# Optimization experiments

Hardware: AMD Instinct MI355X
Metric: run time of the kernel (lower is better)

The kernel has to match this reference:

```python
import math
import jax, jax.numpy as jnp
import numpy as np

D_MODEL = 512
N_HEADS = 8
FACTOR = 1
B, L = 16, 2048


def setup_inputs() -> dict:
    key = jax.random.key(0)
    ks = jax.random.split(key, 12)
    d = D_MODEL
    inp = {
        'queries': jax.random.normal(ks[0], (B, L, d), dtype=jnp.float32),
        'keys':    jax.random.normal(ks[1], (B, L, d), dtype=jnp.float32),
        'values':  jax.random.normal(ks[2], (B, L, d), dtype=jnp.float32),
        # projection params (nn.Linear: y = x @ W.T + b)
        'Wq': jax.random.normal(ks[3], (d, d), dtype=jnp.float32) * 0.02,
        'bq': jnp.zeros((d,), dtype=jnp.float32),
        'Wk': jax.random.normal(ks[4], (d, d), dtype=jnp.float32) * 0.02,
        'bk': jnp.zeros((d,), dtype=jnp.float32),
        'Wv': jax.random.normal(ks[5], (d, d), dtype=jnp.float32) * 0.02,
        'bv': jnp.zeros((d,), dtype=jnp.float32),
        'Wo': jax.random.normal(ks[6], (d, d), dtype=jnp.float32) * 0.02,
        'bo': jnp.zeros((d,), dtype=jnp.float32),
    }
    return inp


def _autocorrelation(q, k, v):
    # q, k, v: [B, H, E, L]
    length = q.shape[-1]
    q_fft = jnp.fft.rfft(q, axis=-1)
    k_fft = jnp.fft.rfft(k, axis=-1)
    corr = jnp.fft.irfft(q_fft * jnp.conj(k_fft), n=length, axis=-1)  # [B,H,E,L]

    # time_delay_agg_training
    top_k = int(FACTOR * math.log(length))  # static
    mean_value = corr.mean(axis=(1, 2))            # [B, L]
    _, index = jax.lax.top_k(mean_value.mean(axis=0), top_k)  # [k], batch-shared delays
    weights = mean_value[:, index]                 # [B, k]
    tmp_corr = jax.nn.softmax(weights, axis=-1)    # [B, k]

    # roll(values, -delay) == values[..., (arange(L)+delay) % L]
    idx = (jnp.arange(length)[None, :] + index[:, None]) % length  # [k, L]
    patterns = v[..., idx]                         # [B, H, E, k, L]
    delays_agg = jnp.einsum('bhekl,bk->bhel', patterns, tmp_corr)  # [B,H,E,L]
    return delays_agg


def reference(queries, keys, values, Wq, bq, Wk, bk, Wv, bv, Wo, bo):
    Bb, Ll, d = queries.shape
    H = N_HEADS
    E = d // H
    # projections, then [B, L, H, E] -> [B, H, E, L]
    q = (queries @ Wq.T + bq).reshape(Bb, Ll, H, E).transpose(0, 2, 3, 1)
    k = (keys    @ Wk.T + bk).reshape(Bb, Ll, H, E).transpose(0, 2, 3, 1)
    v = (values  @ Wv.T + bv).reshape(Bb, Ll, H, E).transpose(0, 2, 3, 1)

    agg = _autocorrelation(q, k, v)                 # [B, H, E, L]
    out = agg.transpose(0, 3, 1, 2).reshape(Bb, Ll, H * E)  # [B, L, d]
    return out @ Wo.T + bo
```

## Files before the change

kernel.cpp:

```cpp
#include <hip/hip_runtime.h>


typedef _Float16 f16;
typedef _Float16 f16x8 __attribute__((ext_vector_type(8)));
typedef _Float16 f16x4 __attribute__((ext_vector_type(4)));
typedef float    f32x4 __attribute__((ext_vector_type(4)));

#define PSI(i) ((i) + ((i) >> 3))
#define TWI(j) ((j) + ((j) >> 4))

__device__ __forceinline__ float2 f2add(float2 a, float2 b) { return make_float2(a.x + b.x, a.y + b.y); }
__device__ __forceinline__ float2 f2sub(float2 a, float2 b) { return make_float2(a.x - b.x, a.y - b.y); }
__device__ __forceinline__ float2 cmul(float2 a, float2 b)  { return make_float2(a.x * b.x - a.y * b.y, a.x * b.y + a.y * b.x); }

__global__ __launch_bounds__(256) void cvt_inputs(
    const float* __restrict__ q, const float* __restrict__ k, const float* __restrict__ v,
    f16* __restrict__ xq, f16* __restrict__ xk, f16* __restrict__ xv)
{
    const float* src = (blockIdx.y == 0) ? q : (blockIdx.y == 1) ? k : v;
    f16*         dst = (blockIdx.y == 0) ? xq : (blockIdx.y == 1) ? xk : xv;
    const int i = blockIdx.x * 256 + threadIdx.x;
    float4 a = ((const float4*)src)[2 * i];
    float4 b = ((const float4*)src)[2 * i + 1];
    f16x8 h = { (f16)a.x, (f16)a.y, (f16)a.z, (f16)a.w,
                (f16)b.x, (f16)b.y, (f16)b.z, (f16)b.w };
    ((f16x8*)dst)[i] = h;
}

__global__ __launch_bounds__(256) void cvt_weights(
    const float* __restrict__ w0, const float* __restrict__ w1,
    const float* __restrict__ w2, const float* __restrict__ w3,
    f16* __restrict__ o0, f16* __restrict__ o1, f16* __restrict__ o2, f16* __restrict__ o3)
{
    const float* src = (blockIdx.y == 0) ? w0 : (blockIdx.y == 1) ? w1 : (blockIdx.y == 2) ? w2 : w3;
    f16*         dst = (blockIdx.y == 0) ? o0 : (blockIdx.y == 1) ? o1 : (blockIdx.y == 2) ? o2 : o3;
    const int i = blockIdx.x * 256 + threadIdx.x;
    float4 val = ((const float4*)src)[i];
    f16x4 h = { (f16)val.x, (f16)val.y, (f16)val.z, (f16)val.w };
    ((f16x4*)dst)[i] = h;
}

__device__ __forceinline__ void stage_op256(const f16* __restrict__ G, int row0, int k0,
                                            f16* __restrict__ lds, int tid)
{
#pragma unroll
    for (int q = 0; q < 4; ++q) {
        const int r = q * 64 + (tid >> 3);
        const int u = (tid & 7) ^ ((tid >> 3) & 7);
        const f16* g = G + (size_t)(row0 + r) * 512 + k0 + u * 8;
        f16* d = lds + q * 4096 + (tid >> 6) * 512;
        __builtin_amdgcn_global_load_lds(
            (const __attribute__((address_space(1))) void*)g,
            (__attribute__((address_space(3))) void*)d, 16, 0, 0);
    }
}

template<int F16OUT, int MT_L2, int NT_L2, int SWZ, int SPLITB>
__global__ __launch_bounds__(512, 2) void gemm_nt(
    const f16* __restrict__ A0, const f16* __restrict__ B0, const f16* __restrict__ B1,
    void* __restrict__ Cout, int N,
    const float* __restrict__ bias_q, const float* __restrict__ bias_k,
    const float* __restrict__ bias_col)
{
    constexpr int BM = 256, BN = 256, NKT = 8;
    constexpr int ESZ = F16OUT ? 2 : 4;

    __shared__ __align__(16) char smem[131072];
    f16* smA = (f16*)smem;
    f16* smB = (f16*)smem + 2 * BM * 64;

    const int tid  = threadIdx.x;
    const int wave = tid >> 6, lane = tid & 63;

    int mt, nt;
    if (SWZ == 1) {
        const int xcd = blockIdx.x & 7, slot = blockIdx.x >> 3;
        mt = slot & ((1 << MT_L2) - 1);
        nt = (xcd << (NT_L2 - 3)) | (slot >> MT_L2);
    } else if (SWZ == 2) {
        const int xcd = blockIdx.x & 7, slot = blockIdx.x >> 3;
        nt = slot & ((1 << NT_L2) - 1);
        mt = (xcd << (MT_L2 - 3)) | (slot >> NT_L2);
    } else {
        nt = blockIdx.x & ((1 << NT_L2) - 1);
        mt = blockIdx.x >> NT_L2;
    }
    const int m0 = mt * BM, n0 = nt * BN;

    const bool useB1 = SPLITB && (mt >= (1 << (MT_L2 - 1)));
    const f16* Bg = useB1 ? B1 : B0;
    const float* brow = SPLITB
        ? (useB1 ? bias_k - (1 << (MT_L2 - 1)) * BM : bias_q)
        : bias_q;

    f32x4 acc[8][4];
#pragma unroll
    for (int m = 0; m < 8; ++m)
#pragma unroll
        for (int n = 0; n < 4; ++n) acc[m][n] = (f32x4){0.f, 0.f, 0.f, 0.f};

    const int fr = lane & 15;
    const int kg = (lane >> 4) * 8;
    const int rowm = fr & 7;
    const int wr = wave >> 2;
    const int wc = wave & 3;
    const int warow = wr * 128 + fr;
    const int wbrow = wc * 64 + fr;

    auto compute = [&](const f16* __restrict__ Ab, const f16* __restrict__ Bb) {
#pragma unroll
        for (int k2 = 0; k2 < 2; ++k2) {
            const int kb = k2 * 32 + kg;
            const int col = ((kb >> 3) ^ rowm) << 3;
            f16x8 af[8], bf[4];
#pragma unroll
            for (int m = 0; m < 8; ++m) af[m] = *(const f16x8*)&Ab[(warow + m * 16) * 64 + col];
#pragma unroll
            for (int n = 0; n < 4; ++n) bf[n] = *(const f16x8*)&Bb[(wbrow + n * 16) * 64 + col];
#pragma unroll
            for (int m = 0; m < 8; ++m)
#pragma unroll
                for (int n = 0; n < 4; ++n)
                    acc[m][n] = __builtin_amdgcn_mfma_f32_16x16x32_f16(af[m], bf[n], acc[m][n], 0, 0, 0);
        }
    };

    stage_op256(A0, m0, 0, smA, tid);
    stage_op256(Bg, n0, 0, smB, tid);
    asm volatile("s_waitcnt vmcnt(0)" ::: "memory");
    __builtin_amdgcn_s_barrier();

#pragma unroll 1
    for (int kk = 0; kk < NKT; ++kk) {
        const int cur = kk & 1;
        if (kk < NKT - 1) {
            stage_op256(A0, m0, (kk + 1) * 64, smA + (cur ^ 1) * BM * 64, tid);
            stage_op256(Bg, n0, (kk + 1) * 64, smB + (cur ^ 1) * BN * 64, tid);
        }
        compute(smA + cur * BM * 64, smB + cur * BN * 64);
        asm volatile("s_waitcnt vmcnt(0) lgkmcnt(0)" ::: "memory");
        __builtin_amdgcn_s_barrier();
    }

    constexpr int L     = F16OUT ? 3 : 2;
    constexpr int CPR   = (BN * ESZ) / 16;
    constexpr int HROWS = F16OUT ? 256 : 128;
    constexpr int NH    = F16OUT ? 1 : 2;
#pragma unroll 1
    for (int h = 0; h < NH; ++h) {
        __syncthreads();
        if (F16OUT || wr == h) {
            const int lr0 = wr * 128 + ((lane >> 4) << 2);
#pragma unroll
            for (int m = 0; m < 8; ++m)
#pragma unroll
                for (int n = 0; n < 4; ++n) {
                    const int col = wc * 64 + n * 16 + fr;
                    const float bc = bias_col ? bias_col[n0 + col] : 0.f;
#pragma unroll
                    for (int j = 0; j < 4; ++j) {
                        const int row  = lr0 + m * 16 + j;
                        const int rl   = row - h * HROWS * (F16OUT ? 0 : 1);
                        const int scol = ((((col >> L) ^ (row & 7)) << L) | (col & ((1 << L) - 1)));
                        float v = acc[m][n][j] + bc + (brow ? brow[m0 + row] : 0.f);
                        if (F16OUT) ((f16*)smem)[row * BN + scol] = (f16)v;
                        else        ((float*)smem)[rl * BN + scol] = v;
                    }
                }
        }
        __syncthreads();
        const int chunks = HROWS * CPR;
#pragma unroll 1
        for (int i = tid; i < chunks; i += 512) {
            const int rl  = i / CPR;
            const int u   = i % CPR;
            const int row = h * HROWS + rl;
            int4 vv = *(const int4*)(smem + (rl * CPR + (u ^ (row & 7))) * 16);
            *(int4*)((char*)Cout + ((size_t)(m0 + row) * N + n0) * ESZ + u * 16) = vv;
        }
    }
}

template<int S>
__device__ __forceinline__ void fft_pass2(float2* __restrict__ z, const float2* __restrict__ tw, int tid)
{
    constexpr int m = 1024 >> S;
    constexpr int h = m >> 1;
#pragma unroll
    for (int rep = 0; rep < 2; ++rep) {
        const int idx = tid + rep * 256;
        const int j2  = idx & (h - 1);
        const int blk = idx >> (9 - S);
        const int i   = (blk << (11 - S)) + j2;
        const float2 w1 = tw[TWI(j2 << S)];
        const float2 w2 = tw[TWI(j2 << (S + 1))];
        float2 a = z[PSI(i)], b = z[PSI(i + h)], c = z[PSI(i + m)], d = z[PSI(i + m + h)];
        float2 a1 = f2add(a, c);
        float2 c1 = cmul(f2sub(a, c), w1);
        float2 b1 = f2add(b, d);
        float2 t0 = cmul(f2sub(b, d), w1);
        float2 d1 = make_float2(t0.y, -t0.x);
        z[PSI(i)]         = f2add(a1, b1);
        z[PSI(i + h)]     = cmul(f2sub(a1, b1), w2);
        z[PSI(i + m)]     = f2add(c1, d1);
        z[PSI(i + m + h)] = cmul(f2sub(c1, d1), w2);
    }
    __syncthreads();
}

__device__ __forceinline__ void fft_tail_scatter(float2* __restrict__ z, int tid)
{
    float2 v[8];
    const int p0 = tid * 8;
#pragma unroll
    for (int e = 0; e < 8; ++e) v[e] = z[PSI(p0 + e)];
    __syncthreads();
    constexpr float RS = 0.70710678118654752f;
    const float2 W8[4] = { {1.f, 0.f}, {RS, -RS}, {0.f, -1.f}, {-RS, -RS} };
#pragma unroll
    for (int e = 0; e < 4; ++e) {
        float2 t = f2sub(v[e], v[e + 4]);
        v[e]     = f2add(v[e], v[e + 4]);
        v[e + 4] = cmul(t, W8[e]);
    }
#pragma unroll
    for (int base = 0; base < 8; base += 4) {
        float2 t0 = f2sub(v[base], v[base + 2]);
        v[base]     = f2add(v[base], v[base + 2]);
        v[base + 2] = t0;
        float2 t1 = f2sub(v[base + 1], v[base + 3]);
        v[base + 1] = f2add(v[base + 1], v[base + 3]);
        v[base + 3] = make_float2(t1.y, -t1.x);
    }
#pragma unroll
    for (int base = 0; base < 8; base += 2) {
        float2 t = f2sub(v[base], v[base + 1]);
        v[base]     = f2add(v[base], v[base + 1]);
        v[base + 1] = t;
    }
    const int br8t = (int)(__brev((unsigned)tid) >> 24);
    const int BR3[8] = {0, 4, 2, 6, 1, 5, 3, 7};
#pragma unroll
    for (int e = 0; e < 8; ++e) {
        const int f = br8t + (BR3[e] << 8);
        z[PSI(f)] = v[e];
    }
    __syncthreads();
}

__device__ __forceinline__ void fft2048_natural(float2* __restrict__ z, const float2* __restrict__ tw, int tid)
{
    fft_pass2<0>(z, tw, tid);
    fft_pass2<2>(z, tw, tid);
    fft_pass2<4>(z, tw, tid);
    fft_pass2<6>(z, tw, tid);
    fft_tail_scatter(z, tid);
}

__device__ __forceinline__ void fill_tw(float2* __restrict__ tw, int tid)
{
    for (int j = tid; j < 1024; j += 256) {
        float sv, cv;
        sincospif(-(float)j * (1.0f / 1024.0f), &sv, &cv);
        tw[TWI(j)] = make_float2(cv, sv);
    }
}

__global__ __launch_bounds__(256) void fft_corr(
    const f16* __restrict__ Qt, const f16* __restrict__ Kt,
    float2* __restrict__ Sp)
{
    __shared__ float2 z[2304];
    __shared__ float2 tw[1088];
    const int tid = threadIdx.x;
    const int grp = blockIdx.x;
    const int b   = blockIdx.y;

    fill_tw(tw, tid);
    float2 racc[5];
#pragma unroll
    for (int r = 0; r < 5; ++r) racc[r] = make_float2(0.f, 0.f);
    __syncthreads();

    for (int ch = 0; ch < 8; ++ch) {
        const int c = grp * 8 + ch;
        const f16x8* qr = (const f16x8*)(Qt + ((size_t)c * 16 + b) * 2048);
        const f16x8* kr = (const f16x8*)(Kt + ((size_t)c * 16 + b) * 2048);
        f16x8 qv = qr[tid], kv = kr[tid];
        const int e0 = tid * 8;
#pragma unroll
        for (int j = 0; j < 8; ++j)
            z[PSI(e0 + j)] = make_float2((float)qv[j], (float)kv[j]);
        __syncthreads();
        fft2048_natural(z, tw, tid);
#pragma unroll
        for (int r = 0; r < 5; ++r) {
            const int f = tid + (r << 8);
            if (f <= 1024) {
                const int pf = (2048 - f) & 2047;
                float2 Zf  = z[PSI(f)];
                float2 Zc0 = z[PSI(pf)];
                float qx = 0.5f * (Zf.x + Zc0.x), qy = 0.5f * (Zf.y - Zc0.y);
                float dx = Zf.x - Zc0.x,          dy = Zf.y + Zc0.y;
                float kx = 0.5f * dy,             ky = -0.5f * dx;
                racc[r].x += qx * kx + qy * ky;
                racc[r].y += qy * kx - qx * ky;
            }
        }
        __syncthreads();
    }
    float2* out = Sp + ((size_t)b * 64 + grp) * 1025;
#pragma unroll
    for (int r = 0; r < 5; ++r) {
        const int f = tid + (r << 8);
        if (f <= 1024) out[f] = racc[r];
    }
}

__global__ __launch_bounds__(256) void reduce_sp(
    const float2* __restrict__ Sp, float2* __restrict__ Sred)
{
    const int b = blockIdx.x;
    const int f = blockIdx.y * 256 + threadIdx.x;
    if (f > 1024) return;
    const float2* base = Sp + (size_t)b * 64 * 1025 + f;
    float sx = 0.f, sy = 0.f;
#pragma unroll 8
    for (int g = 0; g < 64; ++g) {
        float2 p = base[(size_t)g * 1025];
        sx += p.x; sy += p.y;
    }
    Sred[b * 1025 + f] = make_float2(sx, sy);
}

__global__ __launch_bounds__(256) void ifft_mean(
    const float2* __restrict__ Sred, float* __restrict__ mv)
{
    __shared__ float2 z[2304];
    __shared__ float2 tw[1088];
    const int tid = threadIdx.x;
    const int b   = blockIdx.x;
    fill_tw(tw, tid);
#pragma unroll
    for (int r = 0; r < 5; ++r) {
        const int f = tid + (r << 8);
        if (f <= 1024) {
            float2 s = Sred[b * 1025 + f];
            z[PSI(f)] = make_float2(s.x, -s.y);
            if (f >= 1 && f <= 1023)
                z[PSI(2048 - f)] = make_float2(s.x, s.y);
        }
    }
    __syncthreads();
    fft2048_natural(z, tw, tid);
    const float scale = 1.0f / (2048.0f * 512.0f);
    for (int t = tid; t < 2048; t += 256)
        mv[(size_t)b * 2048 + t] = z[PSI(t)].x * scale;
}

__global__ __launch_bounds__(256) void select_topk(
    const float* __restrict__ mv, int* __restrict__ sel, float* __restrict__ wsm)
{
    __shared__ float u[2048];
    __shared__ float rv[256];
    __shared__ int   ri[256];
    __shared__ int   ssel[7];
    const int tid = threadIdx.x;
    for (int t = tid; t < 2048; t += 256) {
        float s = 0.f;
        for (int b = 0; b < 16; ++b) s += mv[b * 2048 + t];
        u[t] = s;
    }
    __syncthreads();
    for (int k = 0; k < 7; ++k) {
        float best = -3.4e38f; int bi = 0x7fffffff;
        for (int t = tid; t < 2048; t += 256)
            if (u[t] > best) { best = u[t]; bi = t; }
        rv[tid] = best; ri[tid] = bi;
        __syncthreads();
        for (int off = 128; off > 0; off >>= 1) {
            if (tid < off) {
                if (rv[tid + off] > rv[tid] ||
                    (rv[tid + off] == rv[tid] && ri[tid + off] < ri[tid])) {
                    rv[tid] = rv[tid + off]; ri[tid] = ri[tid + off];
                }
            }
            __syncthreads();
        }
        if (tid == 0) { ssel[k] = ri[0]; sel[k] = ri[0]; u[ri[0]] = -3.4e38f; }
        __syncthreads();
    }
    if (tid < 16) {
        float vals[7], mx = -3.4e38f;
        for (int k = 0; k < 7; ++k) { vals[k] = mv[tid * 2048 + ssel[k]]; mx = fmaxf(mx, vals[k]); }
        float se = 0.f;
        for (int k = 0; k < 7; ++k) { vals[k] = expf(vals[k] - mx); se += vals[k]; }
        for (int k = 0; k < 7; ++k) wsm[tid * 7 + k] = vals[k] / se;
    }
}

__global__ __launch_bounds__(256) void aggregate(
    const f16* __restrict__ V, const int* __restrict__ sel,
    const float* __restrict__ wsm, f16* __restrict__ agg)
{
    __shared__ int   sidx[7];
    __shared__ float sw[7];
    const int bl = blockIdx.x;
    const int b = bl >> 11, l = bl & 2047;
    if (threadIdx.x < 7) { sidx[threadIdx.x] = sel[threadIdx.x]; sw[threadIdx.x] = wsm[b * 7 + threadIdx.x]; }
    __syncthreads();
    const int c = threadIdx.x;
    float a0 = 0.f, a1 = 0.f;
#pragma unroll
    for (int k = 0; k < 7; ++k) {
        const int lk = (l + sidx[k]) & 2047;
        const f16* row = V + ((size_t)b * 2048 + lk) * 512;
        a0 += sw[k] * (float)row[c];
        a1 += sw[k] * (float)row[c + 256];
    }
    f16* orow = agg + ((size_t)b * 2048 + l) * 512;
    orow[c]       = (f16)a0;
    orow[c + 256] = (f16)a1;
}

extern "C" void kernel_launch(void* const* d_in, const int* in_sizes, int n_in,
                              void* d_out, int out_size, void* d_ws, size_t ws_size,
                              hipStream_t stream)
{
    (void)in_sizes; (void)n_in; (void)out_size; (void)ws_size;
    const float* queries = (const float*)d_in[0];
    const float* keys    = (const float*)d_in[1];
    const float* values  = (const float*)d_in[2];
    const float* Wq = (const float*)d_in[3];
    const float* bq = (const float*)d_in[4];
    const float* Wk = (const float*)d_in[5];
    const float* bk = (const float*)d_in[6];
    const float* Wv = (const float*)d_in[7];
    const float* bv = (const float*)d_in[8];
    const float* Wo = (const float*)d_in[9];
    const float* bo = (const float*)d_in[10];

    char* p = (char*)d_ws;
    f16*    Xq  = (f16*)p;    p += 33554432;
    f16*    Xk  = (f16*)p;    p += 33554432;
    f16*    Xv  = (f16*)p;    p += 33554432;
    f16*    QKt = (f16*)p;    p += 67108864;
    f16*    Vb  = (f16*)p;    p += 33554432;
    f16*    agg = (f16*)p;    p += 33554432;
    f16*    wqh = (f16*)p;    p += 524288;
    f16*    wkh = (f16*)p;    p += 524288;
    f16*    wvh = (f16*)p;    p += 524288;
    f16*    woh = (f16*)p;    p += 524288;
    float2* Sp  = (float2*)p; p += 8396800;
    float2* Srd = (float2*)p; p += 131200;
    float*  mv  = (float*)p;  p += 131072;
    int*    sel = (int*)p;    p += 256;
    float*  wsm = (float*)p;  p += 512;
    f16*    Kt  = QKt + (size_t)512 * 32768;

    cvt_weights<<<dim3(256, 4), 256, 0, stream>>>(Wq, Wk, Wv, Wo, wqh, wkh, wvh, woh);
    cvt_inputs<<<dim3(8192, 3), 256, 0, stream>>>(queries, keys, values, Xq, Xk, Xv);

    gemm_nt<1, 2, 7, 1, 1><<<512, 512, 0, stream>>>(
        wqh, Xq, Xk, QKt, 32768, bq, bk, nullptr);

    gemm_nt<1, 7, 1, 2, 0><<<256, 512, 0, stream>>>(
        Xv, wvh, nullptr, Vb, 512, nullptr, nullptr, bv);

    fft_corr<<<dim3(64, 16), 256, 0, stream>>>(QKt, Kt, Sp);
    reduce_sp<<<dim3(16, 5), 256, 0, stream>>>(Sp, Srd);
    ifft_mean<<<16, 256, 0, stream>>>(Srd, mv);
    select_topk<<<1, 256, 0, stream>>>(mv, sel, wsm);
    aggregate<<<32768, 256, 0, stream>>>(Vb, sel, wsm, agg);

    gemm_nt<0, 7, 1, 2, 0><<<256, 512, 0, stream>>>(
        agg, woh, nullptr, (float*)d_out, 512, nullptr, nullptr, bo);
}
```

Baseline: 318.4 us.

## Fuse fp32-to-fp16 input conversion into projection GEMM operand loading

```diff
diff --git a/kernel.cpp b/kernel.cpp
--- a/kernel.cpp
+++ b/kernel.cpp
@@ -12,20 +12,6 @@
 __device__ __forceinline__ float2 f2add(float2 a, float2 b) { return make_float2(a.x + b.x, a.y + b.y); }
 __device__ __forceinline__ float2 f2sub(float2 a, float2 b) { return make_float2(a.x - b.x, a.y - b.y); }
 __device__ __forceinline__ float2 cmul(float2 a, float2 b)  { return make_float2(a.x * b.x - a.y * b.y, a.x * b.y + a.y * b.x); }
-
-__global__ __launch_bounds__(256) void cvt_inputs(
-    const float* __restrict__ q, const float* __restrict__ k, const float* __restrict__ v,
-    f16* __restrict__ xq, f16* __restrict__ xk, f16* __restrict__ xv)
-{
-    const float* src = (blockIdx.y == 0) ? q : (blockIdx.y == 1) ? k : v;
-    f16*         dst = (blockIdx.y == 0) ? xq : (blockIdx.y == 1) ? xk : xv;
-    const int i = blockIdx.x * 256 + threadIdx.x;
-    float4 a = ((const float4*)src)[2 * i];
-    float4 b = ((const float4*)src)[2 * i + 1];
-    f16x8 h = { (f16)a.x, (f16)a.y, (f16)a.z, (f16)a.w,
-                (f16)b.x, (f16)b.y, (f16)b.z, (f16)b.w };
-    ((f16x8*)dst)[i] = h;
-}
 
 __global__ __launch_bounds__(256) void cvt_weights(
     const float* __restrict__ w0, const float* __restrict__ w1,
@@ -40,8 +26,8 @@
     ((f16x4*)dst)[i] = h;
 }
 
-__device__ __forceinline__ void stage_op256(const f16* __restrict__ G, int row0, int k0,
-                                            f16* __restrict__ lds, int tid)
+__device__ __forceinline__ void stage_f16(const f16* __restrict__ G, int row0, int k0,
+                                          f16* __restrict__ lds, int tid)
 {
 #pragma unroll
     for (int q = 0; q < 4; ++q) {
@@ -55,9 +41,32 @@
     }
 }
 
-template<int F16OUT, int MT_L2, int NT_L2, int SWZ, int SPLITB>
+__device__ __forceinline__ void load_f32_slab(const float* __restrict__ G, int row0, int k0,
+                                              int tid, float4* __restrict__ rg)
+{
+#pragma unroll
+    for (int q = 0; q < 4; ++q) {
+        const float* g = G + (size_t)(row0 + q * 64 + (tid >> 3)) * 512 + k0 + (tid & 7) * 8;
+        rg[2 * q]     = *(const float4*)g;
+        rg[2 * q + 1] = *(const float4*)(g + 4);
+    }
+}
+__device__ __forceinline__ void write_f16_slab(f16* __restrict__ lds, int tid,
+                                               const float4* __restrict__ rg)
+{
+#pragma unroll
+    for (int q = 0; q < 4; ++q) {
+        float4 a = rg[2 * q], b = rg[2 * q + 1];
+        f16x8 h = { (f16)a.x, (f16)a.y, (f16)a.z, (f16)a.w,
+                    (f16)b.x, (f16)b.y, (f16)b.z, (f16)b.w };
+        const int uu = (tid & 7) ^ ((tid >> 3) & 7);
+        *(f16x8*)(lds + q * 4096 + (tid >> 3) * 64 + (uu << 3)) = h;
+    }
+}
+
+template<int AF32, int BF32, int F16OUT, int MT_L2, int NT_L2, int SWZ, int SPLITB>
 __global__ __launch_bounds__(512, 2) void gemm_nt(
-    const f16* __restrict__ A0, const f16* __restrict__ B0, const f16* __restrict__ B1,
+    const void* __restrict__ A0v, const void* __restrict__ B0v, const void* __restrict__ B1v,
     void* __restrict__ Cout, int N,
     const float* __restrict__ bias_q, const float* __restrict__ bias_k,
     const float* __restrict__ bias_col)
@@ -88,10 +97,15 @@
     const int m0 = mt * BM, n0 = nt * BN;
 
     const bool useB1 = SPLITB && (mt >= (1 << (MT_L2 - 1)));
-    const f16* Bg = useB1 ? B1 : B0;
+    const void* Bgv = useB1 ? B1v : B0v;
     const float* brow = SPLITB
         ? (useB1 ? bias_k - (1 << (MT_L2 - 1)) * BM : bias_q)
         : bias_q;
+
+    const f16*   Ah = (const f16*)A0v;
+    const float* Af = (const float*)A0v;
+    const f16*   Bh = (const f16*)Bgv;
+    const float* Bf = (const float*)Bgv;
 
     f32x4 acc[8][4];
 #pragma unroll
@@ -125,19 +139,30 @@
         }
     };
 
-    stage_op256(A0, m0, 0, smA, tid);
-    stage_op256(Bg, n0, 0, smB, tid);
-    asm volatile("s_waitcnt vmcnt(0)" ::: "memory");
+    float4 ra[8], rb[8];
+
+    if (AF32) { load_f32_slab(Af, m0, 0, tid, ra); write_f16_slab(smA, tid, ra); }
+    else      stage_f16(Ah, m0, 0, smA, tid);
+    if (BF32) { load_f32_slab(Bf, n0, 0, tid, rb); write_f16_slab(smB, tid, rb); }
+    else      stage_f16(Bh, n0, 0, smB, tid);
+    asm volatile("s_waitcnt vmcnt(0) lgkmcnt(0)" ::: "memory");
     __builtin_amdgcn_s_barrier();
 
 #pragma unroll 1
     for (int kk = 0; kk < NKT; ++kk) {
         const int cur = kk & 1;
         if (kk < NKT - 1) {
-            stage_op256(A0, m0, (kk + 1) * 64, smA + (cur ^ 1) * BM * 64, tid);
-            stage_op256(Bg, n0, (kk + 1) * 64, smB + (cur ^ 1) * BN * 64, tid);
+            const int k0 = (kk + 1) * 64;
+            if (AF32) load_f32_slab(Af, m0, k0, tid, ra);
+            else      stage_f16(Ah, m0, k0, smA + (cur ^ 1) * BM * 64, tid);
+            if (BF32) load_f32_slab(Bf, n0, k0, tid, rb);
+            else      stage_f16(Bh, n0, k0, smB + (cur ^ 1) * BN * 64, tid);
         }
         compute(smA + cur * BM * 64, smB + cur * BN * 64);
+        if (kk < NKT - 1) {
+            if (AF32) write_f16_slab(smA + (cur ^ 1) * BM * 64, tid, ra);
+            if (BF32) write_f16_slab(smB + (cur ^ 1) * BN * 64, tid, rb);
+        }
         asm volatile("s_waitcnt vmcnt(0) lgkmcnt(0)" ::: "memory");
         __builtin_amdgcn_s_barrier();
     }
@@ -441,9 +466,6 @@
     const float* bo = (const float*)d_in[10];
 
     char* p = (char*)d_ws;
-    f16*    Xq  = (f16*)p;    p += 33554432;
-    f16*    Xk  = (f16*)p;    p += 33554432;
-    f16*    Xv  = (f16*)p;    p += 33554432;
     f16*    QKt = (f16*)p;    p += 67108864;
     f16*    Vb  = (f16*)p;    p += 33554432;
     f16*    agg = (f16*)p;    p += 33554432;
@@ -459,13 +481,12 @@
     f16*    Kt  = QKt + (size_t)512 * 32768;
 
     cvt_weights<<<dim3(256, 4), 256, 0, stream>>>(Wq, Wk, Wv, Wo, wqh, wkh, wvh, woh);
-    cvt_inputs<<<dim3(8192, 3), 256, 0, stream>>>(queries, keys, values, Xq, Xk, Xv);
-
-    gemm_nt<1, 2, 7, 1, 1><<<512, 512, 0, stream>>>(
-        wqh, Xq, Xk, QKt, 32768, bq, bk, nullptr);
-
-    gemm_nt<1, 7, 1, 2, 0><<<256, 512, 0, stream>>>(
-        Xv, wvh, nullptr, Vb, 512, nullptr, nullptr, bv);
+
+    gemm_nt<0, 1, 1, 2, 7, 1, 1><<<512, 512, 0, stream>>>(
+        wqh, queries, keys, QKt, 32768, bq, bk, nullptr);
+
+    gemm_nt<1, 0, 1, 7, 1, 2, 0><<<256, 512, 0, stream>>>(
+        values, wvh, nullptr, Vb, 512, nullptr, nullptr, bv);
 
     fft_corr<<<dim3(64, 16), 256, 0, stream>>>(QKt, Kt, Sp);
     reduce_sp<<<dim3(16, 5), 256, 0, stream>>>(Sp, Srd);
@@ -473,6 +494,6 @@
     select_topk<<<1, 256, 0, stream>>>(mv, sel, wsm);
     aggregate<<<32768, 256, 0, stream>>>(Vb, sel, wsm, agg);
 
-    gemm_nt<0, 7, 1, 2, 0><<<256, 512, 0, stream>>>(
+    gemm_nt<0, 0, 0, 7, 1, 2, 0><<<256, 512, 0, stream>>>(
         agg, woh, nullptr, (float*)d_out, 512, nullptr, nullptr, bo);
 }
```

Result: faster. 285.7 us (-10.3%).
